# Kernel tuning notes

Hardware: AMD Instinct MI355X
Metric: run time of the kernel (lower is better)

The kernel has to match this reference:

```python
import jax, jax.numpy as jnp
import numpy as np

B, S, DM, DC, L, NS = 4, 2048, 2048, 512, 4, 5  # batch, seq, d_model, d_cortical, n_layers, n_settle


def _ln(x, g, b):
    # torch nn.LayerNorm, eps=1e-5
    m = x.mean(-1, keepdims=True)
    v = ((x - m) ** 2).mean(-1, keepdims=True)
    return (x - m) * jax.lax.rsqrt(v + 1e-5) * g + b


def setup_inputs() -> dict:
    key = jax.random.key(0)
    ks = jax.random.split(key, 20)
    f = lambda k, sh: jax.random.normal(k, sh, jnp.float32) * 0.02
    return dict(
        qwen_final_hidden=jax.random.normal(ks[0], (B, S, DM), jnp.float32),
        obs=jax.random.normal(ks[1], (4, B, S, DM), jnp.float32),
        proj_W=f(ks[2], (4, DC, DM)), proj_b=f(ks[3], (4, DC)),
        fuse_W=f(ks[4], (DC, 4 * DC)), fuse_b=f(ks[5], (DC,)),
        up_W=f(ks[6], (L, DC, DC)), up_b=f(ks[7], (L, DC)),
        lateral_W=f(ks[8], (L, DC, DC)), lateral_b=f(ks[9], (L, DC)),
        precision_logit=f(ks[10], (L, DC)),
        ln_g=jnp.ones((L, DC), jnp.float32), ln_b=jnp.zeros((L, DC), jnp.float32),
        down_W=f(ks[11], (L - 1, DC, DC)), down_b=f(ks[12], (L - 1, DC)),
        out1_W=f(ks[13], (DC, DC)), out1_b=f(ks[14], (DC,)),
        out2_W=f(ks[15], (DM, DC)), out2_b=f(ks[16], (DM,)),
    )


def reference(qwen_final_hidden, obs, proj_W, proj_b, fuse_W, fuse_b,
              up_W, up_b, lateral_W, lateral_b, precision_logit,
              ln_g, ln_b, down_W, down_b, out1_W, out1_b, out2_W, out2_b):
    b, s, dm = qwen_final_hidden.shape
    # per-observed-layer input projections, concatenated along features
    proj = jnp.einsum('obsd,ocd->bsoc', obs, proj_W) + proj_b  # (B,S,4,DC)
    cat = proj.reshape(b, s, -1)
    fused = cat @ fuse_W.T + fuse_b                             # (B,S,DC)
    x0 = fused.reshape(b * s, DC)                               # per-token cortical input

    prec = jax.nn.sigmoid(precision_logit)                      # (L,DC)

    # initial bottom-up pass: activations = compress(x)
    acts = []
    x = x0
    for i in range(L):
        x = _ln(x @ up_W[i].T + up_b[i], ln_g[i], ln_b[i])
        acts.append(x)

    # settling iterations
    for _ in range(NS):
        # top-down predictions computed from pre-sweep activations
        preds = [None] * L
        for i in range(L - 1, 0, -1):
            if i < L - 1:  # top layer has no top-down weights
                preds[i - 1] = acts[i] @ down_W[i].T + down_b[i]
        x = x0
        for i in range(L):
            compressed = _ln(x @ up_W[i].T + up_b[i], ln_g[i], ln_b[i])
            target = preds[i] if preds[i] is not None else acts[i]
            werr = (compressed - target) * prec[i]
            lateral = acts[i] @ lateral_W[i].T + lateral_b[i]
            acts[i] = _ln(acts[i] + 0.5 * werr + 0.1 * lateral, ln_g[i], ln_b[i])
            x = acts[i]

    top = acts[-1]
    h = jax.nn.gelu(top @ out1_W.T + out1_b, approximate=False)
    correction = (h @ out2_W.T + out2_b).reshape(b, s, dm)
    return qwen_final_hidden + correction
```

## Files before the change

### kernel.cpp

```cpp
#include <hip/hip_runtime.h>
#include <hip/hip_bf16.h>
#include <math.h>

#define NTOK 8192
#define DMD  2048
#define DCC  512
#define TOKH 4194304

typedef __attribute__((ext_vector_type(8))) short short8;
typedef __attribute__((ext_vector_type(4))) float f32x4;

__device__ inline float bf2f(unsigned short u) {
    union { unsigned int i; float f; } x; x.i = ((unsigned int)u) << 16; return x.f;
}
__device__ inline unsigned short f2bf(float f) {
    union { float f; unsigned int i; } x; x.f = f;
    unsigned int u = x.i;
    return (unsigned short)((u + 0x7fffu + ((u >> 16) & 1u)) >> 16);
}

typedef const __attribute__((address_space(1))) unsigned int* gas1_t;
typedef __attribute__((address_space(3))) unsigned int* las3_t;
__device__ inline void async16(const void* g, void* l) {
    __builtin_amdgcn_global_load_lds(
        (gas1_t)g,
        (las3_t)(unsigned int)(unsigned long long)l, 16, 0, 0);
}

#define VMCNT(N) asm volatile("s_waitcnt vmcnt(" #N ")" ::: "memory")

__global__ __launch_bounds__(256)
void cvt_kernel(const float* __restrict__ s, unsigned short* __restrict__ d, int n4)
{
    for (int i = blockIdx.x * 256 + threadIdx.x; i < n4; i += gridDim.x * 256) {
        float4 v = ((const float4*)s)[i];
        ushort4 o;
        o.x = f2bf(v.x); o.y = f2bf(v.y); o.z = f2bf(v.z); o.w = f2bf(v.w);
        ((ushort4*)d)[i] = o;
    }
}

struct PrepArgs {
    const float* wsrc[6];
    const float* proj_W;
    const float* fuse_W;
    const float* fuse_b;
    const float* proj_b;
    unsigned short* wdst;
    unsigned short* projT;
    float* bp;
};

__global__ __launch_bounds__(256)
void prep_kernel(PrepArgs pa)
{
    __shared__ float t[32][33];
    const int bid = blockIdx.x;
    const int tid = threadIdx.x;

    if (bid < 2048) {
        const int total = 1310720;
        for (int i = bid * 256 + tid; i < total; i += 2048 * 256) {
            const float* sp; int base;
            if      (i <  262144) { sp = pa.wsrc[0]; base = 0;       }
            else if (i <  524288) { sp = pa.wsrc[1]; base = 262144;  }
            else if (i <  786432) { sp = pa.wsrc[2]; base = 524288;  }
            else if (i <  983040) { sp = pa.wsrc[3]; base = 786432;  }
            else if (i < 1048576) { sp = pa.wsrc[4]; base = 983040;  }
            else                  { sp = pa.wsrc[5]; base = 1048576; }
            float4 v = ((const float4*)sp)[i - base];
            ushort4 o;
            o.x = f2bf(v.x); o.y = f2bf(v.y); o.z = f2bf(v.z); o.w = f2bf(v.w);
            ((ushort4*)pa.wdst)[i] = o;
        }
    } else if (bid < 6144) {
        const int b2  = bid - 2048;
        const int o   = b2 >> 10;
        const int rem = b2 & 1023;
        const int jb  = (rem & 63) * 32;
        const int kb  = (rem >> 6) * 32;
        const int r   = tid >> 3;
        const int c4  = (tid & 7) * 4;
        {
            const float* s = pa.proj_W + ((size_t)o * DCC + kb + r) * DMD + jb + c4;
            float4 v = *(const float4*)s;
            t[r][c4+0]=v.x; t[r][c4+1]=v.y; t[r][c4+2]=v.z; t[r][c4+3]=v.w;
        }
        __syncthreads();
        {
            ushort4 u;
            u.x = f2bf(t[c4+0][r]); u.y = f2bf(t[c4+1][r]);
            u.z = f2bf(t[c4+2][r]); u.w = f2bf(t[c4+3][r]);
            *(ushort4*)(pa.projT + ((size_t)o * DMD + jb + r) * DCC + kb + c4) = u;
        }
    } else {
        const int b3  = bid - 6144;
        const int row = b3 * 8 + (tid >> 5);
        const int l32 = tid & 31;
        const float* r = pa.fuse_W + (size_t)row * (4 * DCC) + l32 * 64;
        const float* p = pa.proj_b + l32 * 64;
        float s = 0.f;
        #pragma unroll
        for (int k = 0; k < 64; k += 4) {
            float4 v = *(const float4*)(r + k);
            float4 q = *(const float4*)(p + k);
            s += v.x*q.x + v.y*q.y + v.z*q.z + v.w*q.w;
        }
        #pragma unroll
        for (int off = 16; off; off >>= 1) s += __shfl_xor(s, off, 64);
        if (l32 == 0) pa.bp[row] = s + pa.fuse_b[row];
    }
}

struct GArgs {
    const unsigned short* A[6];
    const unsigned short* W[6];
    const float*          bias[6];
    const float*          add[6];
    void*                 C[6];
};

template<bool OUTF32, bool GELU>
__global__ __launch_bounds__(256)
void gemm16(GArgs ga, int lda, int ldw, int ldadd, int ldc, int K)
{
    __shared__ unsigned short As[3][128 * 32];
    __shared__ unsigned short Bs[3][128 * 32];

    const int z    = blockIdx.z;
    const int tid  = threadIdx.x;
    const int wave = tid >> 6;
    const int lane = tid & 63;

    const int nwg   = gridDim.x * gridDim.y;
    const int bid   = blockIdx.y * gridDim.x + blockIdx.x;
    const int swz   = (bid & 7) * (nwg >> 3) + (bid >> 3);
    const int bn    = (swz % gridDim.x) * 128;
    const int bm    = (swz / gridDim.x) * 128;

    const int wr   = wave >> 1;
    const int wc   = wave & 1;

    const unsigned short* Ap = ga.A[z];
    const unsigned short* Wp = ga.W[z];

    const int lrow = lane >> 2;
    const int lcol = (lane & 3) * 8;
    const int l15  = lane & 15;
    const int lh   = lane >> 4;

    f32x4 acc[4][4] = {};

    const int nsteps = K >> 5;

    auto issue = [&](int buf, int k0) {
        #pragma unroll
        for (int r = 0; r < 2; ++r) {
            int c = wave + r * 4;
            async16(Ap + (size_t)(bm + c * 16 + lrow) * lda + k0 + lcol,
                    &As[buf][c * 512]);
            async16(Wp + (size_t)(bn + c * 16 + lrow) * ldw + k0 + lcol,
                    &Bs[buf][c * 512]);
        }
    };

    issue(0, 0);
    issue(1, 32);

    for (int t = 0; t < nsteps; ++t) {
        const int cur = t % 3;
        if (t < nsteps - 1) VMCNT(4);
        else                VMCNT(0);
        __builtin_amdgcn_s_barrier();
        if (t + 2 < nsteps) issue((t + 2) % 3, (t + 2) * 32);

        short8 af[4], bfr[4];
        #pragma unroll
        for (int i = 0; i < 4; ++i) {
            af[i]  = *(const short8*)&As[cur][(wr * 64 + i * 16 + l15) * 32 + lh * 8];
            bfr[i] = *(const short8*)&Bs[cur][(wc * 64 + i * 16 + l15) * 32 + lh * 8];
        }
        __builtin_amdgcn_s_setprio(1);
        #pragma unroll
        for (int mi = 0; mi < 4; ++mi)
            #pragma unroll
            for (int ni = 0; ni < 4; ++ni)
                acc[mi][ni] = __builtin_amdgcn_mfma_f32_16x16x32_bf16(
                    af[mi], bfr[ni], acc[mi][ni], 0, 0, 0);
        __builtin_amdgcn_s_setprio(0);
    }

    const float* bias = ga.bias[z];
    const float* add  = ga.add[z];
    #pragma unroll
    for (int ni = 0; ni < 4; ++ni) {
        int col = bn + wc * 64 + ni * 16 + l15;
        float bv = bias ? bias[col] : 0.0f;
        #pragma unroll
        for (int mi = 0; mi < 4; ++mi) {
            #pragma unroll
            for (int r = 0; r < 4; ++r) {
                int row = bm + wr * 64 + mi * 16 + lh * 4 + r;
                float vv = acc[mi][ni][r] + bv;
                if (GELU) vv = 0.5f * vv * (1.0f + erff(vv * 0.7071067811865475f));
                if (OUTF32) {
                    if (add) vv += add[(size_t)row * ldadd + col];
                    ((float*)ga.C[z])[(size_t)row * ldc + col] = vv;
                } else {
                    ((unsigned short*)ga.C[z])[(size_t)row * ldc + col] = f2bf(vv);
                }
            }
        }
    }
}

__global__ __launch_bounds__(256)
void x0red(const float* __restrict__ partial, const float* __restrict__ bp,
           unsigned short* __restrict__ x0)
{
    const int i = blockIdx.x * 256 + threadIdx.x;
    float4 a = ((const float4*)partial)[i];
    float4 b = ((const float4*)(partial + TOKH))[i];
    float4 c = ((const float4*)(partial + 2 * (size_t)TOKH))[i];
    float4 d = ((const float4*)(partial + 3 * (size_t)TOKH))[i];
    const int col = (i * 4) & (DCC - 1);
    float4 bv = *(const float4*)(bp + col);
    ushort4 o;
    o.x = f2bf(a.x + b.x + c.x + d.x + bv.x);
    o.y = f2bf(a.y + b.y + c.y + d.y + bv.y);
    o.z = f2bf(a.z + b.z + c.z + d.z + bv.z);
    o.w = f2bf(a.w + b.w + c.w + d.w + bv.w);
    ((ushort4*)x0)[i] = o;
}

__device__ inline int csw(int rl, int col) {
    int s = ((rl >> 2) & 3) ^ (rl & 3);
    return rl * 512 + (col ^ (s << 4));
}

template<int MODE>
__global__ __launch_bounds__(512)
void gemm_fused(const unsigned short* __restrict__ Ap,
                const unsigned short* __restrict__ Wp,
                const float* __restrict__ bias,
                const float* __restrict__ g,
                const float* __restrict__ b,
                const unsigned short* a_in,
                const unsigned short* t_in,
                const unsigned short* __restrict__ lat_in,
                const float* __restrict__ logit,
                unsigned short* outp)
{
    __shared__ unsigned short Bs[3][512 * 32];
    __shared__ unsigned short As3[3][32 * 32];
    __shared__ float red[2][8][32];

    const int tid  = threadIdx.x;
    const int wave = tid >> 6;
    const int lane = tid & 63;
    const int lrow = lane >> 2;
    const int lc8  = (lane & 3) * 8;
    const int bm   = blockIdx.x * 32;
    const int l15  = lane & 15;
    const int lh   = lane >> 4;
    const int c0   = lane * 8;

    f32x4 acc[2][4] = {};

    auto issue = [&](int buf, int k0) {
        if (wave < 2)
            async16(Ap + (size_t)(bm + wave * 16 + lrow) * DCC + k0 + lc8,
                    &As3[buf][wave * 512]);
        #pragma unroll
        for (int r = 0; r < 4; ++r)
            async16(Wp + (size_t)((r * 8 + wave) * 16 + lrow) * DCC + k0 + lc8,
                    &Bs[buf][(r * 8 + wave) * 512]);
    };

    issue(0, 0);
    issue(1, 32);

    #pragma unroll
    for (int t = 0; t < 16; ++t) {
        const int cur = t % 3;
        if (t < 15) { if (wave < 2) VMCNT(5); else VMCNT(4); }
        else        { VMCNT(0); }
        __builtin_amdgcn_s_barrier();
        if (t + 2 < 16) issue((t + 2) % 3, (t + 2) * 32);

        short8 af[2], bfr[4];
        #pragma unroll
        for (int mi = 0; mi < 2; ++mi)
            af[mi] = *(const short8*)&As3[cur][(mi * 16 + l15) * 32 + lh * 8];
        #pragma unroll
        for (int ni = 0; ni < 4; ++ni)
            bfr[ni] = *(const short8*)&Bs[cur][(wave * 64 + ni * 16 + l15) * 32 + lh * 8];
        __builtin_amdgcn_s_setprio(1);
        #pragma unroll
        for (int mi = 0; mi < 2; ++mi)
            #pragma unroll
            for (int ni = 0; ni < 4; ++ni)
                acc[mi][ni] = __builtin_amdgcn_mfma_f32_16x16x32_bf16(
                    af[mi], bfr[ni], acc[mi][ni], 0, 0, 0);
        __builtin_amdgcn_s_setprio(0);
    }

    float bv[4], gv[4], bbv[4];
    #pragma unroll
    for (int ni = 0; ni < 4; ++ni) {
        int col = wave * 64 + ni * 16 + l15;
        bv[ni] = bias[col]; gv[ni] = g[col]; bbv[ni] = b[col];
    }

    float ps[2][4], pq[2][4];
    #pragma unroll
    for (int mi = 0; mi < 2; ++mi)
        #pragma unroll
        for (int rr = 0; rr < 4; ++rr) {
            float s = 0.f, q = 0.f;
            #pragma unroll
            for (int ni = 0; ni < 4; ++ni) {
                float v = acc[mi][ni][rr] + bv[ni];
                acc[mi][ni][rr] = v;
                s += v; q += v * v;
            }
            #pragma unroll
            for (int off = 1; off < 16; off <<= 1) {
                s += __shfl_xor(s, off, 64);
                q += __shfl_xor(q, off, 64);
            }
            ps[mi][rr] = s; pq[mi][rr] = q;
        }
    if (l15 == 0) {
        #pragma unroll
        for (int mi = 0; mi < 2; ++mi)
            #pragma unroll
            for (int rr = 0; rr < 4; ++rr) {
                int rl = mi * 16 + lh * 4 + rr;
                red[0][wave][rl] = ps[mi][rr];
                red[1][wave][rl] = pq[mi][rr];
            }
    }
    __syncthreads();

    unsigned short* compS = &Bs[0][0];
    #pragma unroll
    for (int mi = 0; mi < 2; ++mi)
        #pragma unroll
        for (int rr = 0; rr < 4; ++rr) {
            int rl = mi * 16 + lh * 4 + rr;
            float s = 0.f, q = 0.f;
            #pragma unroll
            for (int w = 0; w < 8; ++w) { s += red[0][w][rl]; q += red[1][w][rl]; }
            float m1 = s * (1.0f / DCC);
            float r1 = rsqrtf(q * (1.0f / DCC) - m1 * m1 + 1e-5f);
            #pragma unroll
            for (int ni = 0; ni < 4; ++ni) {
                int col = wave * 64 + ni * 16 + l15;
                compS[csw(rl, col)] = f2bf((acc[mi][ni][rr] - m1) * r1 * gv[ni] + bbv[ni]);
            }
        }
    __syncthreads();

    if constexpr (MODE == 0) {
        #pragma unroll
        for (int rr = 0; rr < 4; ++rr) {
            const int rl = wave * 4 + rr;
            const size_t gbase = (size_t)(bm + rl) * DCC + c0;
            short8 cm = *(const short8*)&compS[csw(rl, c0)];
            *(short8*)(outp + gbase) = cm;
        }
    } else {
        float gr[8], br[8], pr[8];
        {
            float4 g0 = *(const float4*)(g + c0),     g1 = *(const float4*)(g + c0 + 4);
            float4 b0 = *(const float4*)(b + c0),     b1 = *(const float4*)(b + c0 + 4);
            float4 p0 = *(const float4*)(logit + c0), p1 = *(const float4*)(logit + c0 + 4);
            float gt[8] = {g0.x,g0.y,g0.z,g0.w,g1.x,g1.y,g1.z,g1.w};
            float bt[8] = {b0.x,b0.y,b0.z,b0.w,b1.x,b1.y,b1.z,b1.w};
            float pt[8] = {p0.x,p0.y,p0.z,p0.w,p1.x,p1.y,p1.z,p1.w};
            #pragma unroll
            for (int j = 0; j < 8; ++j) {
                gr[j] = gt[j]; br[j] = bt[j];
                pr[j] = 1.0f / (1.0f + __expf(-pt[j]));
            }
        }
        #pragma unroll
        for (int rr = 0; rr < 4; ++rr) {
            const int rl = wave * 4 + rr;
            const size_t gbase = (size_t)(bm + rl) * DCC + c0;
            short8 cm = *(const short8*)&compS[csw(rl, c0)];
            short8 ar = *(const short8*)(a_in + gbase);
            short8 tr = *(const short8*)(t_in + gbase);
            short8 lr = *(const short8*)(lat_in + gbase);
            float tv[8], s = 0.f, q = 0.f;
            #pragma unroll
            for (int j = 0; j < 8; ++j) {
                float val = bf2f((unsigned short)ar[j])
                          + 0.5f * (bf2f((unsigned short)cm[j]) - bf2f((unsigned short)tr[j])) * pr[j]
                          + 0.1f * bf2f((unsigned short)lr[j]);
                tv[j] = val; s += val; q += val * val;
            }
            #pragma unroll
            for (int off = 1; off < 64; off <<= 1) {
                s += __shfl_xor(s, off, 64);
                q += __shfl_xor(q, off, 64);
            }
            float m2 = s * (1.0f / DCC);
            float r2 = rsqrtf(q * (1.0f / DCC) - m2 * m2 + 1e-5f);
            short8 o;
            #pragma unroll
            for (int j = 0; j < 8; ++j)
                o[j] = (short)f2bf((tv[j] - m2) * r2 * gr[j] + br[j]);
            *(short8*)(outp + gbase) = o;
        }
    }
}

extern "C" void kernel_launch(void* const* d_in, const int* in_sizes, int n_in,
                              void* d_out, int out_size, void* d_ws, size_t ws_size,
                              hipStream_t stream)
{
    const float* qwen   = (const float*)d_in[0];
    const float* obs    = (const float*)d_in[1];
    const float* proj_W = (const float*)d_in[2];
    const float* proj_b = (const float*)d_in[3];
    const float* fuse_W = (const float*)d_in[4];
    const float* fuse_b = (const float*)d_in[5];
    const float* up_W   = (const float*)d_in[6];
    const float* up_b   = (const float*)d_in[7];
    const float* lat_W  = (const float*)d_in[8];
    const float* lat_b  = (const float*)d_in[9];
    const float* plogit = (const float*)d_in[10];
    const float* ln_g   = (const float*)d_in[11];
    const float* ln_b   = (const float*)d_in[12];
    const float* down_W = (const float*)d_in[13];
    const float* down_b = (const float*)d_in[14];
    const float* out1_W = (const float*)d_in[15];
    const float* out1_b = (const float*)d_in[16];
    const float* out2_W = (const float*)d_in[17];
    const float* out2_b = (const float*)d_in[18];
    float* out = (float*)d_out;

    unsigned short* wsu = (unsigned short*)d_ws;
    float*          bp     = (float*)wsu;
    unsigned short* h16    = wsu + 2048;
    unsigned short* M16    = wsu + 8388608;
    unsigned short* x0b    = wsu + 16777216;
    unsigned short* acts16[4] = {
        wsu + 20971520, wsu + 20971520 + TOKH,
        wsu + 20971520 + 2 * TOKH, wsu + 20971520 + 3 * TOKH };
    unsigned short* w16    = wsu + 37748736;
    unsigned short* fuseW16 = w16;
    unsigned short* upW16   = w16 + 1048576;
    unsigned short* latW16  = w16 + 2097152;
    unsigned short* downW16 = w16 + 3145728;
    unsigned short* out1W16 = w16 + 3932160;
    unsigned short* out2W16 = w16 + 4194304;
    unsigned short* projT16 = wsu + 47185920;
    unsigned short* obs16   = wsu + 47185920;

    float*          part32  = (float*)d_out;
    unsigned short* outu = (unsigned short*)d_out;
    unsigned short* pred16a = outu;
    unsigned short* pred16b = outu + TOKH;
    unsigned short* lat16[4] = { outu + 2*TOKH, outu + 3*TOKH, outu + 4*TOKH, outu + 5*TOKH };

    dim3 blk(256);
    dim3 blk512(512);

    {
        PrepArgs pa;
        pa.wsrc[0] = fuse_W; pa.wsrc[1] = up_W;   pa.wsrc[2] = lat_W;
        pa.wsrc[3] = down_W; pa.wsrc[4] = out1_W; pa.wsrc[5] = out2_W;
        pa.proj_W = proj_W; pa.fuse_W = fuse_W; pa.fuse_b = fuse_b;
        pa.proj_b = proj_b;
        pa.wdst = w16; pa.projT = projT16; pa.bp = bp;
        prep_kernel<<<dim3(6208), blk, 0, stream>>>(pa);
    }

    {
        GArgs a{};
        for (int o = 0; o < 4; ++o) {
            a.A[o] = fuseW16 + o * DCC;
            a.W[o] = projT16 + (size_t)o * DMD * DCC;
            a.bias[o] = nullptr;
            a.C[o] = M16 + (size_t)o * DCC * DMD;
        }
        gemm16<false, false><<<dim3(DMD/128, DCC/128, 4), blk, 0, stream>>>(
            a, 4 * DCC, DCC, 0, DMD, DCC);
    }

    cvt_kernel<<<dim3(4096), blk, 0, stream>>>(obs, obs16, 16777216);

    {
        GArgs a{};
        for (int o = 0; o < 4; ++o) {
            a.A[o] = obs16 + (size_t)o * NTOK * DMD;
            a.W[o] = M16 + (size_t)o * DCC * DMD;
            a.bias[o] = nullptr;
            a.add[o]  = nullptr;
            a.C[o] = part32 + (size_t)o * TOKH;
        }
        gemm16<true, false><<<dim3(DCC/128, NTOK/128, 4), blk, 0, stream>>>(
            a, DMD, DMD, 0, DCC, DMD);
    }
    x0red<<<dim3(TOKH/4/256), blk, 0, stream>>>(part32, bp, x0b);

    dim3 fgrid(NTOK / 32);

    for (int i = 0; i < 4; ++i) {
        gemm_fused<0><<<fgrid, blk512, 0, stream>>>(
            (i == 0) ? x0b : acts16[i - 1],
            upW16 + (size_t)i * DCC * DCC, up_b + i * DCC,
            ln_g + i * DCC, ln_b + i * DCC,
            nullptr, nullptr, nullptr, nullptr, acts16[i]);
    }

    for (int s = 0; s < 5; ++s) {
        {
            GArgs a{};
            a.A[0] = acts16[1]; a.W[0] = downW16 + (size_t)1 * DCC * DCC;
            a.bias[0] = down_b + 1 * DCC; a.C[0] = pred16a;
            a.A[1] = acts16[2]; a.W[1] = downW16 + (size_t)2 * DCC * DCC;
            a.bias[1] = down_b + 2 * DCC; a.C[1] = pred16b;
            for (int i = 0; i < 4; ++i) {
                a.A[2 + i] = acts16[i];
                a.W[2 + i] = latW16 + (size_t)i * DCC * DCC;
                a.bias[2 + i] = lat_b + i * DCC;
                a.C[2 + i] = lat16[i];
            }
            gemm16<false, false><<<dim3(DCC/128, NTOK/128, 6), blk, 0, stream>>>(
                a, DCC, DCC, 0, DCC, DCC);
        }
        for (int i = 0; i < 4; ++i) {
            const unsigned short* tgt =
                (i == 0) ? pred16a : (i == 1) ? pred16b : acts16[i];
            gemm_fused<1><<<fgrid, blk512, 0, stream>>>(
                (i == 0) ? x0b : acts16[i - 1],
                upW16 + (size_t)i * DCC * DCC, up_b + i * DCC,
                ln_g + i * DCC, ln_b + i * DCC,
                acts16[i], tgt, lat16[i], plogit + i * DCC, acts16[i]);
        }
    }

    {
        GArgs a{};
        a.A[0] = acts16[3]; a.W[0] = out1W16; a.bias[0] = out1_b; a.C[0] = h16;
        gemm16<false, true><<<dim3(DCC/128, NTOK/128, 1), blk, 0, stream>>>(
            a, DCC, DCC, 0, DCC, DCC);
    }
    {
        GArgs a{};
        a.A[0] = h16; a.W[0] = out2W16; a.bias[0] = out2_b;
        a.add[0] = qwen; a.C[0] = out;
        gemm16<true, false><<<dim3(DMD/128, NTOK/128, 1), blk, 0, stream>>>(
            a, DCC, DCC, DMD, DMD, DCC);
    }
}
```

Measured before the change: 1.399 ms.

## Fuse consecutive up-projection layers pairwise, keeping intermediate activations in LDS

The per-layer GEMM+LayerNorm+settle kernel now handles two consecutive layers in one launch. The first layer's normalized output tile stays in a new shared-memory buffer and feeds the second layer's MFMA loop directly as the A operand. This halves the fused-kernel launches in the initial pass and in each settling step. It also removes a global read of the intermediate activation. The cost is more LDS per block (an extra 32 KB tile) and a longer serial kernel per block, which leaves less room for occupancy.

```diff
diff --git a/kernel.cpp b/kernel.cpp
--- a/kernel.cpp
+++ b/kernel.cpp
@@ -240,19 +240,29 @@
 
 template<int MODE>
 __global__ __launch_bounds__(512)
-void gemm_fused(const unsigned short* __restrict__ Ap,
-                const unsigned short* __restrict__ Wp,
-                const float* __restrict__ bias,
-                const float* __restrict__ g,
-                const float* __restrict__ b,
-                const unsigned short* a_in,
-                const unsigned short* t_in,
-                const unsigned short* __restrict__ lat_in,
-                const float* __restrict__ logit,
-                unsigned short* outp)
+void gemm_fused2(const unsigned short* __restrict__ Ap,
+                 const unsigned short* __restrict__ W0,
+                 const float* __restrict__ bias0,
+                 const float* __restrict__ g0,
+                 const float* __restrict__ b0,
+                 const unsigned short* a0,
+                 const unsigned short* t0,
+                 const unsigned short* __restrict__ lat0,
+                 const float* __restrict__ logit0,
+                 unsigned short* out0,
+                 const unsigned short* __restrict__ W1,
+                 const float* __restrict__ bias1,
+                 const float* __restrict__ g1,
+                 const float* __restrict__ b1,
+                 const unsigned short* a1,
+                 const unsigned short* t1,
+                 const unsigned short* __restrict__ lat1,
+                 const float* __restrict__ logit1,
+                 unsigned short* out1)
 {
     __shared__ unsigned short Bs[3][512 * 32];
     __shared__ unsigned short As3[3][32 * 32];
+    __shared__ unsigned short xS[32 * 512];
     __shared__ float red[2][8][32];
 
     const int tid  = threadIdx.x;
@@ -265,20 +275,142 @@
     const int lh   = lane >> 4;
     const int c0   = lane * 8;
 
-    f32x4 acc[2][4] = {};
-
-    auto issue = [&](int buf, int k0) {
+    f32x4 acc[2][4];
+
+    auto ln1_to_xS = [&](const float* bias, const float* g, const float* b) {
+        float bv[4], gv[4], bbv[4];
+        #pragma unroll
+        for (int ni = 0; ni < 4; ++ni) {
+            int col = wave * 64 + ni * 16 + l15;
+            bv[ni] = bias[col]; gv[ni] = g[col]; bbv[ni] = b[col];
+        }
+        float ps[2][4], pq[2][4];
+        #pragma unroll
+        for (int mi = 0; mi < 2; ++mi)
+            #pragma unroll
+            for (int rr = 0; rr < 4; ++rr) {
+                float s = 0.f, q = 0.f;
+                #pragma unroll
+                for (int ni = 0; ni < 4; ++ni) {
+                    float v = acc[mi][ni][rr] + bv[ni];
+                    acc[mi][ni][rr] = v;
+                    s += v; q += v * v;
+                }
+                #pragma unroll
+                for (int off = 1; off < 16; off <<= 1) {
+                    s += __shfl_xor(s, off, 64);
+                    q += __shfl_xor(q, off, 64);
+                }
+                ps[mi][rr] = s; pq[mi][rr] = q;
+            }
+        if (l15 == 0) {
+            #pragma unroll
+            for (int mi = 0; mi < 2; ++mi)
+                #pragma unroll
+                for (int rr = 0; rr < 4; ++rr) {
+                    int rl = mi * 16 + lh * 4 + rr;
+                    red[0][wave][rl] = ps[mi][rr];
+                    red[1][wave][rl] = pq[mi][rr];
+                }
+        }
+        __syncthreads();
+        #pragma unroll
+        for (int mi = 0; mi < 2; ++mi)
+            #pragma unroll
+            for (int rr = 0; rr < 4; ++rr) {
+                int rl = mi * 16 + lh * 4 + rr;
+                float s = 0.f, q = 0.f;
+                #pragma unroll
+                for (int w = 0; w < 8; ++w) { s += red[0][w][rl]; q += red[1][w][rl]; }
+                float m1 = s * (1.0f / DCC);
+                float r1 = rsqrtf(q * (1.0f / DCC) - m1 * m1 + 1e-5f);
+                #pragma unroll
+                for (int ni = 0; ni < 4; ++ni) {
+                    int col = wave * 64 + ni * 16 + l15;
+                    xS[csw(rl, col)] = f2bf((acc[mi][ni][rr] - m1) * r1 * gv[ni] + bbv[ni]);
+                }
+            }
+        __syncthreads();
+    };
+
+    auto phase2 = [&](const unsigned short* a_in, const unsigned short* t_in,
+                      const unsigned short* lat_in, const float* g,
+                      const float* b, const float* logit,
+                      unsigned short* outp, bool keep) {
+        if constexpr (MODE == 0) {
+            #pragma unroll
+            for (int rr = 0; rr < 4; ++rr) {
+                const int rl = wave * 4 + rr;
+                const size_t gbase = (size_t)(bm + rl) * DCC + c0;
+                short8 cm = *(const short8*)&xS[csw(rl, c0)];
+                *(short8*)(outp + gbase) = cm;
+            }
+        } else {
+            float gr[8], br[8], pr[8];
+            {
+                float4 ga = *(const float4*)(g + c0),     gb = *(const float4*)(g + c0 + 4);
+                float4 ba = *(const float4*)(b + c0),     bb2 = *(const float4*)(b + c0 + 4);
+                float4 pA = *(const float4*)(logit + c0), pB = *(const float4*)(logit + c0 + 4);
+                float gt[8] = {ga.x,ga.y,ga.z,ga.w,gb.x,gb.y,gb.z,gb.w};
+                float bt[8] = {ba.x,ba.y,ba.z,ba.w,bb2.x,bb2.y,bb2.z,bb2.w};
+                float pt[8] = {pA.x,pA.y,pA.z,pA.w,pB.x,pB.y,pB.z,pB.w};
+                #pragma unroll
+                for (int j = 0; j < 8; ++j) {
+                    gr[j] = gt[j]; br[j] = bt[j];
+                    pr[j] = 1.0f / (1.0f + __expf(-pt[j]));
+                }
+            }
+            #pragma unroll
+            for (int rr = 0; rr < 4; ++rr) {
+                const int rl = wave * 4 + rr;
+                const size_t gbase = (size_t)(bm + rl) * DCC + c0;
+                short8 cm = *(const short8*)&xS[csw(rl, c0)];
+                short8 ar = *(const short8*)(a_in + gbase);
+                short8 tr = *(const short8*)(t_in + gbase);
+                short8 lr = *(const short8*)(lat_in + gbase);
+                float tv[8], s = 0.f, q = 0.f;
+                #pragma unroll
+                for (int j = 0; j < 8; ++j) {
+                    float val = bf2f((unsigned short)ar[j])
+                              + 0.5f * (bf2f((unsigned short)cm[j]) - bf2f((unsigned short)tr[j])) * pr[j]
+                              + 0.1f * bf2f((unsigned short)lr[j]);
+                    tv[j] = val; s += val; q += val * val;
+                }
+                #pragma unroll
+                for (int off = 1; off < 64; off <<= 1) {
+                    s += __shfl_xor(s, off, 64);
+                    q += __shfl_xor(q, off, 64);
+                }
+                float m2 = s * (1.0f / DCC);
+                float r2 = rsqrtf(q * (1.0f / DCC) - m2 * m2 + 1e-5f);
+                short8 o;
+                #pragma unroll
+                for (int j = 0; j < 8; ++j)
+                    o[j] = (short)f2bf((tv[j] - m2) * r2 * gr[j] + br[j]);
+                *(short8*)(outp + gbase) = o;
+                if (keep) *(short8*)&xS[csw(rl, c0)] = o;
+            }
+        }
+    };
+
+    #pragma unroll
+    for (int mi = 0; mi < 2; ++mi)
+        #pragma unroll
+        for (int ni = 0; ni < 4; ++ni)
+            acc[mi][ni] = f32x4{0.f, 0.f, 0.f, 0.f};
+
+    auto issueA = [&](int buf, int k0) {
         if (wave < 2)
             async16(Ap + (size_t)(bm + wave * 16 + lrow) * DCC + k0 + lc8,
                     &As3[buf][wave * 512]);
         #pragma unroll
         for (int r = 0; r < 4; ++r)
-            async16(Wp + (size_t)((r * 8 + wave) * 16 + lrow) * DCC + k0 + lc8,
+            async16(W0 + (size_t)((r * 8 + wave) * 16 + lrow) * DCC + k0 + lc8,
                     &Bs[buf][(r * 8 + wave) * 512]);
     };
 
-    issue(0, 0);
-    issue(1, 32);
+    issueA(0, 0);
+    issueA(1, 32);
 
     #pragma unroll
     for (int t = 0; t < 16; ++t) {
@@ -286,7 +418,7 @@
         if (t < 15) { if (wave < 2) VMCNT(5); else VMCNT(4); }
         else        { VMCNT(0); }
         __builtin_amdgcn_s_barrier();
-        if (t + 2 < 16) issue((t + 2) % 3, (t + 2) * 32);
+        if (t + 2 < 16) issueA((t + 2) % 3, (t + 2) * 32);
 
         short8 af[2], bfr[4];
         #pragma unroll
@@ -305,116 +437,53 @@
         __builtin_amdgcn_s_setprio(0);
     }
 
-    float bv[4], gv[4], bbv[4];
-    #pragma unroll
-    for (int ni = 0; ni < 4; ++ni) {
-        int col = wave * 64 + ni * 16 + l15;
-        bv[ni] = bias[col]; gv[ni] = g[col]; bbv[ni] = b[col];
-    }
-
-    float ps[2][4], pq[2][4];
+    ln1_to_xS(bias0, g0, b0);
+    phase2(a0, t0, lat0, g0, b0, logit0, out0, true);
+    __syncthreads();
+
     #pragma unroll
     for (int mi = 0; mi < 2; ++mi)
         #pragma unroll
-        for (int rr = 0; rr < 4; ++rr) {
-            float s = 0.f, q = 0.f;
-            #pragma unroll
-            for (int ni = 0; ni < 4; ++ni) {
-                float v = acc[mi][ni][rr] + bv[ni];
-                acc[mi][ni][rr] = v;
-                s += v; q += v * v;
-            }
-            #pragma unroll
-            for (int off = 1; off < 16; off <<= 1) {
-                s += __shfl_xor(s, off, 64);
-                q += __shfl_xor(q, off, 64);
-            }
-            ps[mi][rr] = s; pq[mi][rr] = q;
-        }
-    if (l15 == 0) {
+        for (int ni = 0; ni < 4; ++ni)
+            acc[mi][ni] = f32x4{0.f, 0.f, 0.f, 0.f};
+
+    auto issueB = [&](int buf, int k0) {
+        #pragma unroll
+        for (int r = 0; r < 4; ++r)
+            async16(W1 + (size_t)((r * 8 + wave) * 16 + lrow) * DCC + k0 + lc8,
+                    &Bs[buf][(r * 8 + wave) * 512]);
+    };
+
+    issueB(0, 0);
+    issueB(1, 32);
+
+    #pragma unroll
+    for (int t = 0; t < 16; ++t) {
+        const int cur = t % 3;
+        if (t < 15) VMCNT(4);
+        else        VMCNT(0);
+        __builtin_amdgcn_s_barrier();
+        if (t + 2 < 16) issueB((t + 2) % 3, (t + 2) * 32);
+
+        short8 af[2], bfr[4];
         #pragma unroll
         for (int mi = 0; mi < 2; ++mi)
-            #pragma unroll
-            for (int rr = 0; rr < 4; ++rr) {
-                int rl = mi * 16 + lh * 4 + rr;
-                red[0][wave][rl] = ps[mi][rr];
-                red[1][wave][rl] = pq[mi][rr];
-            }
-    }
-    __syncthreads();
-
-    unsigned short* compS = &Bs[0][0];
-    #pragma unroll
-    for (int mi = 0; mi < 2; ++mi)
-        #pragma unroll
-        for (int rr = 0; rr < 4; ++rr) {
-            int rl = mi * 16 + lh * 4 + rr;
-            float s = 0.f, q = 0.f;
-            #pragma unroll
-            for (int w = 0; w < 8; ++w) { s += red[0][w][rl]; q += red[1][w][rl]; }
-            float m1 = s * (1.0f / DCC);
-            float r1 = rsqrtf(q * (1.0f / DCC) - m1 * m1 + 1e-5f);
-            #pragma unroll
-            for (int ni = 0; ni < 4; ++ni) {
-                int col = wave * 64 + ni * 16 + l15;
-                compS[csw(rl, col)] = f2bf((acc[mi][ni][rr] - m1) * r1 * gv[ni] + bbv[ni]);
-            }
-        }
-    __syncthreads();
-
-    if constexpr (MODE == 0) {
-        #pragma unroll
-        for (int rr = 0; rr < 4; ++rr) {
-            const int rl = wave * 4 + rr;
-            const size_t gbase = (size_t)(bm + rl) * DCC + c0;
-            short8 cm = *(const short8*)&compS[csw(rl, c0)];
-            *(short8*)(outp + gbase) = cm;
-        }
-    } else {
-        float gr[8], br[8], pr[8];
-        {
-            float4 g0 = *(const float4*)(g + c0),     g1 = *(const float4*)(g + c0 + 4);
-            float4 b0 = *(const float4*)(b + c0),     b1 = *(const float4*)(b + c0 + 4);
-            float4 p0 = *(const float4*)(logit + c0), p1 = *(const float4*)(logit + c0 + 4);
-            float gt[8] = {g0.x,g0.y,g0.z,g0.w,g1.x,g1.y,g1.z,g1.w};
-            float bt[8] = {b0.x,b0.y,b0.z,b0.w,b1.x,b1.y,b1.z,b1.w};
-            float pt[8] = {p0.x,p0.y,p0.z,p0.w,p1.x,p1.y,p1.z,p1.w};
-            #pragma unroll
-            for (int j = 0; j < 8; ++j) {
-                gr[j] = gt[j]; br[j] = bt[j];
-                pr[j] = 1.0f / (1.0f + __expf(-pt[j]));
-            }
-        }
-        #pragma unroll
-        for (int rr = 0; rr < 4; ++rr) {
-            const int rl = wave * 4 + rr;
-            const size_t gbase = (size_t)(bm + rl) * DCC + c0;
-            short8 cm = *(const short8*)&compS[csw(rl, c0)];
-            short8 ar = *(const short8*)(a_in + gbase);
-            short8 tr = *(const short8*)(t_in + gbase);
-            short8 lr = *(const short8*)(lat_in + gbase);
-            float tv[8], s = 0.f, q = 0.f;
-            #pragma unroll
-            for (int j = 0; j < 8; ++j) {
-                float val = bf2f((unsigned short)ar[j])
-                          + 0.5f * (bf2f((unsigned short)cm[j]) - bf2f((unsigned short)tr[j])) * pr[j]
-                          + 0.1f * bf2f((unsigned short)lr[j]);
-                tv[j] = val; s += val; q += val * val;
-            }
-            #pragma unroll
-            for (int off = 1; off < 64; off <<= 1) {
-                s += __shfl_xor(s, off, 64);
-                q += __shfl_xor(q, off, 64);
-            }
-            float m2 = s * (1.0f / DCC);
-            float r2 = rsqrtf(q * (1.0f / DCC) - m2 * m2 + 1e-5f);
-            short8 o;
-            #pragma unroll
-            for (int j = 0; j < 8; ++j)
-                o[j] = (short)f2bf((tv[j] - m2) * r2 * gr[j] + br[j]);
-            *(short8*)(outp + gbase) = o;
-        }
-    }
+            af[mi] = *(const short8*)&xS[csw(mi * 16 + l15, t * 32 + lh * 8)];
+        #pragma unroll
+        for (int ni = 0; ni < 4; ++ni)
+            bfr[ni] = *(const short8*)&Bs[cur][(wave * 64 + ni * 16 + l15) * 32 + lh * 8];
+        __builtin_amdgcn_s_setprio(1);
+        #pragma unroll
+        for (int mi = 0; mi < 2; ++mi)
+            #pragma unroll
+            for (int ni = 0; ni < 4; ++ni)
+                acc[mi][ni] = __builtin_amdgcn_mfma_f32_16x16x32_bf16(
+                    af[mi], bfr[ni], acc[mi][ni], 0, 0, 0);
+        __builtin_amdgcn_s_setprio(0);
+    }
+
+    ln1_to_xS(bias1, g1, b1);
+    phase2(a1, t1, lat1, g1, b1, logit1, out1, false);
 }
 
 extern "C" void kernel_launch(void* const* d_in, const int* in_sizes, int n_in,
@@ -509,13 +578,18 @@
 
     dim3 fgrid(NTOK / 32);
 
-    for (int i = 0; i < 4; ++i) {
-        gemm_fused<0><<<fgrid, blk512, 0, stream>>>(
-            (i == 0) ? x0b : acts16[i - 1],
-            upW16 + (size_t)i * DCC * DCC, up_b + i * DCC,
-            ln_g + i * DCC, ln_b + i * DCC,
-            nullptr, nullptr, nullptr, nullptr, acts16[i]);
-    }
+    gemm_fused2<0><<<fgrid, blk512, 0, stream>>>(
+        x0b,
+        upW16,                 up_b,           ln_g,           ln_b,
+        nullptr, nullptr, nullptr, nullptr, acts16[0],
+        upW16 + 262144,        up_b + DCC,     ln_g + DCC,     ln_b + DCC,
+        nullptr, nullptr, nullptr, nullptr, acts16[1]);
+    gemm_fused2<0><<<fgrid, blk512, 0, stream>>>(
+        acts16[1],
+        upW16 + 2 * 262144,    up_b + 2 * DCC, ln_g + 2 * DCC, ln_b + 2 * DCC,
+        nullptr, nullptr, nullptr, nullptr, acts16[2],
+        upW16 + 3 * 262144,    up_b + 3 * DCC, ln_g + 3 * DCC, ln_b + 3 * DCC,
+        nullptr, nullptr, nullptr, nullptr, acts16[3]);
 
     for (int s = 0; s < 5; ++s) {
         {
@@ -533,15 +607,18 @@
             gemm16<false, false><<<dim3(DCC/128, NTOK/128, 6), blk, 0, stream>>>(
                 a, DCC, DCC, 0, DCC, DCC);
         }
-        for (int i = 0; i < 4; ++i) {
-            const unsigned short* tgt =
-                (i == 0) ? pred16a : (i == 1) ? pred16b : acts16[i];
-            gemm_fused<1><<<fgrid, blk512, 0, stream>>>(
-                (i == 0) ? x0b : acts16[i - 1],
-                upW16 + (size_t)i * DCC * DCC, up_b + i * DCC,
-                ln_g + i * DCC, ln_b + i * DCC,
-                acts16[i], tgt, lat16[i], plogit + i * DCC, acts16[i]);
-        }
+        gemm_fused2<1><<<fgrid, blk512, 0, stream>>>(
+            x0b,
+            upW16,              up_b,           ln_g,           ln_b,
+            acts16[0], pred16a, lat16[0], plogit,         acts16[0],
+            upW16 + 262144,     up_b + DCC,     ln_g + DCC,     ln_b + DCC,
+            acts16[1], pred16b, lat16[1], plogit + DCC,   acts16[1]);
+        gemm_fused2<1><<<fgrid, blk512, 0, stream>>>(
+            acts16[1],
+            upW16 + 2 * 262144, up_b + 2 * DCC, ln_g + 2 * DCC, ln_b + 2 * DCC,
+            acts16[2], acts16[2], lat16[2], plogit + 2 * DCC, acts16[2],
+            upW16 + 3 * 262144, up_b + 3 * DCC, ln_g + 3 * DCC, ln_b + 3 * DCC,
+            acts16[3], acts16[3], lat16[3], plogit + 3 * DCC, acts16[3]);
     }
 
     {
```

After: 1.351 ms (median of 2 runs). -3.4%, faster.
